# Optimization experiments

Hardware: AMD Instinct MI355X
Metric: run time of the kernel (lower is better)

The kernel has to match this reference:

```python
import jax, jax.numpy as jnp
import numpy as np

# Segmented tensor product, uniform-1d case (subscripts 'u,u,u'):
#   out[z, idx_out[p]*u:(idx_out[p]+1)*u] += coeffs[p] * x0_seg[z, idx0[p]] * x1_seg[z, idx1[p]]
U = 128          # mode extent 'u'
NSEG = (32, 8, 32)  # segments per operand (in0, in1, out)
P = 128          # number of paths
Z = 16384        # batch


def setup_inputs() -> dict:
    key = jax.random.key(0)
    k0, k1, k2, k3, k4, k5 = jax.random.split(key, 6)
    return {
        "x0": jax.random.normal(k0, (Z, NSEG[0] * U), dtype=jnp.float32),
        "x1": jax.random.normal(k1, (Z, NSEG[1] * U), dtype=jnp.float32),
        "coeffs": jax.random.normal(k2, (P,), dtype=jnp.float32),
        "idx0": jax.random.randint(k3, (P,), 0, NSEG[0], dtype=jnp.int32),
        "idx1": jax.random.randint(k4, (P,), 0, NSEG[1], dtype=jnp.int32),
        "idx_out": jax.random.randint(k5, (P,), 0, NSEG[2], dtype=jnp.int32),
    }


def reference(x0, x1, coeffs, idx0, idx1, idx_out):
    z = x0.shape[0]
    x0r = x0.reshape(z, NSEG[0], U)  # [Z, n0, u]
    x1r = x1.reshape(z, NSEG[1], U)  # [Z, n1, u]
    # gather the segment used by each path: [Z, P, u]
    s0 = x0r[:, idx0, :]
    s1 = x1r[:, idx1, :]
    # per-path contribution, elementwise over u (coefficient subscript is scalar)
    contrib = (s0 * s1) * coeffs[None, :, None]          # [Z, P, u]
    # scatter-add paths into output segments
    contrib = jnp.transpose(contrib, (1, 0, 2))          # [P, Z, u]
    out_seg = jax.ops.segment_sum(contrib, idx_out, num_segments=NSEG[2])  # [n2, Z, u]
    return jnp.transpose(out_seg, (1, 0, 2)).reshape(z, NSEG[2] * U)
```

## Files before the change

kernel.cpp:

```cpp
#include <hip/hip_runtime.h>


#define Z_DIM 16384
#define U_DIM 128
#define NSEG0 32
#define NSEG1 8
#define NSEG2 32
#define P_DIM 128
#define ZPB   2
#define BLK   512
#define NBLOCKS 512
#define NTILES  (Z_DIM / ZPB)
#define TILES_PER_BLOCK (NTILES / NBLOCKS)

#define X0_FLOATS (ZPB * NSEG0 * U_DIM)
#define X1_FLOATS (ZPB * NSEG1 * U_DIM)
#define BUF_FLOATS (X0_FLOATS + X1_FLOATS)

typedef float f32x4 __attribute__((ext_vector_type(4)));

__global__ __launch_bounds__(128) void tp_setup(
    const float* __restrict__ coeffs,
    const int* __restrict__ idx0,
    const int* __restrict__ idx1,
    const int* __restrict__ idx_out,
    int* __restrict__ off_g,
    int2* __restrict__ meta_g)
{
    __shared__ int s_cnt[NSEG2];
    __shared__ int s_off[NSEG2 + 1];
    const int t = threadIdx.x;
    if (t < NSEG2) s_cnt[t] = 0;
    __syncthreads();
    const int o = idx_out[t];
    const int r = atomicAdd(&s_cnt[o], 1);
    __syncthreads();
    if (t == 0) {
        int sum = 0;
        for (int i = 0; i < NSEG2; ++i) { s_off[i] = sum; sum += s_cnt[i]; }
        s_off[NSEG2] = sum;
    }
    __syncthreads();
    meta_g[s_off[o] + r] = make_int2((idx0[t] * (U_DIM * 4)) | ((idx1[t] * (U_DIM * 4)) << 16),
                                     __float_as_int(coeffs[t]));
    if (t <= NSEG2) off_g[t] = s_off[t];
}

__device__ __forceinline__ void stage_tile(const float* __restrict__ x0,
                                           const float* __restrict__ x1,
                                           float* lbuf, size_t z0, int t)
{
    const float4* g0 = reinterpret_cast<const float4*>(x0 + z0 * (NSEG0 * U_DIM));
    const float4* g1 = reinterpret_cast<const float4*>(x1 + z0 * (NSEG1 * U_DIM));
    float4* l0 = reinterpret_cast<float4*>(lbuf);
    float4* l1 = reinterpret_cast<float4*>(lbuf + X0_FLOATS);
    #pragma unroll
    for (int i = 0; i < (X0_FLOATS / 4) / BLK; ++i)
        __builtin_amdgcn_global_load_lds(
            (const __attribute__((address_space(1))) void*)(g0 + i * BLK + t),
            (__attribute__((address_space(3))) void*)(l0 + i * BLK + t),
            16, 0, 0);
    __builtin_amdgcn_global_load_lds(
        (const __attribute__((address_space(1))) void*)(g1 + t),
        (__attribute__((address_space(3))) void*)(l1 + t),
        16, 0, 0);
}

__global__ __launch_bounds__(BLK) void tp_kernel(
    const float* __restrict__ x0,
    const float* __restrict__ x1,
    const int* __restrict__ off_g,
    const int2* __restrict__ meta_g,
    float* __restrict__ out)
{
    __shared__ float buf[2][BUF_FLOATS];

    const int t  = threadIdx.x;
    const int w4 = __builtin_amdgcn_readfirstlane(t >> 6) * 4;
    const int zl = (t >> 5) & 1;
    const int uq = t & 31;

    const size_t tile0 = (size_t)blockIdx.x * TILES_PER_BLOCK;

    stage_tile(x0, x1, &buf[0][0], tile0 * ZPB, t);

    int cur = 0;
    for (int i = 0; i < TILES_PER_BLOCK; ++i) {
        __syncthreads();

        if (i + 1 < TILES_PER_BLOCK)
            stage_tile(x0, x1, &buf[cur ^ 1][0], (tile0 + i + 1) * ZPB, t);

        const float* x0base = &buf[cur][zl * (NSEG0 * U_DIM) + uq * 4];
        const float* x1base = &buf[cur][X0_FLOATS + zl * (NSEG1 * U_DIM) + uq * 4];
        const size_t z = (tile0 + i) * ZPB + zl;
        float* orow = out + z * (NSEG2 * U_DIM) + uq * 4;

        #pragma unroll
        for (int oo = 0; oo < 4; ++oo) {
            const int o = w4 + oo;
            const int b = off_g[o];
            const int e = off_g[o + 1];
            f32x4 acc = (f32x4)0.f;
            for (int k = b; k < e; ++k) {
                const int2  m = meta_g[k];
                const float c = __int_as_float(m.y);
                const f32x4 a = *reinterpret_cast<const f32x4*>(
                    reinterpret_cast<const char*>(x0base) + (m.x & 0xffff));
                const f32x4 v = *reinterpret_cast<const f32x4*>(
                    reinterpret_cast<const char*>(x1base) + ((unsigned)m.x >> 16));
                acc += a * v * c;
            }
            __builtin_nontemporal_store(acc, reinterpret_cast<f32x4*>(orow + o * U_DIM));
        }
        cur ^= 1;
    }
}

extern "C" void kernel_launch(void* const* d_in, const int* in_sizes, int n_in,
                              void* d_out, int out_size, void* d_ws, size_t ws_size,
                              hipStream_t stream) {
    const float* x0      = (const float*)d_in[0];
    const float* x1      = (const float*)d_in[1];
    const float* coeffs  = (const float*)d_in[2];
    const int*   idx0    = (const int*)d_in[3];
    const int*   idx1    = (const int*)d_in[4];
    const int*   idx_out = (const int*)d_in[5];
    float* out = (float*)d_out;

    int*  off_g  = (int*)d_ws;
    int2* meta_g = (int2*)((char*)d_ws + 256);

    tp_setup<<<1, P_DIM, 0, stream>>>(coeffs, idx0, idx1, idx_out, off_g, meta_g);
    tp_kernel<<<NBLOCKS, BLK, 0, stream>>>(x0, x1, off_g, meta_g, out);
}
```

Measured before the change: 122.7 us.

## Launch one block per two-row tile and stage path metadata in LDS

Replaces the persistent double-buffered loop (512 blocks each walking 16 tiles) with one 1024-thread block per two-row tile. Each wave now handles two output segments instead of four, and occupancy is left to the hardware scheduler. The setup kernel writes offsets and path metadata into one padded blob, which each block copies into LDS with global_load_lds, so the inner loop reads LDS instead of global memory and prefetches the next metadata entry. The trade is the loss of explicit load/compute overlap within a block, plus a full barrier and a metadata reload in every one of 8192 blocks.

```diff
diff --git a/kernel.cpp b/kernel.cpp
--- a/kernel.cpp
+++ b/kernel.cpp
@@ -8,14 +8,13 @@
 #define NSEG2 32
 #define P_DIM 128
 #define ZPB   2
-#define BLK   512
-#define NBLOCKS 512
-#define NTILES  (Z_DIM / ZPB)
-#define TILES_PER_BLOCK (NTILES / NBLOCKS)
+#define BLK   1024
 
 #define X0_FLOATS (ZPB * NSEG0 * U_DIM)
 #define X1_FLOATS (ZPB * NSEG1 * U_DIM)
-#define BUF_FLOATS (X0_FLOATS + X1_FLOATS)
+
+#define META_BASE 40
+#define BLOB_INTS 304
 
 typedef float f32x4 __attribute__((ext_vector_type(4)));
 
@@ -24,8 +23,7 @@
     const int* __restrict__ idx0,
     const int* __restrict__ idx1,
     const int* __restrict__ idx_out,
-    int* __restrict__ off_g,
-    int2* __restrict__ meta_g)
+    int* __restrict__ blob)
 {
     __shared__ int s_cnt[NSEG2];
     __shared__ int s_off[NSEG2 + 1];
@@ -41,79 +39,80 @@
         s_off[NSEG2] = sum;
     }
     __syncthreads();
-    meta_g[s_off[o] + r] = make_int2((idx0[t] * (U_DIM * 4)) | ((idx1[t] * (U_DIM * 4)) << 16),
-                                     __float_as_int(coeffs[t]));
-    if (t <= NSEG2) off_g[t] = s_off[t];
+    const int d = s_off[o] + r;
+    int2* meta = reinterpret_cast<int2*>(blob + META_BASE);
+    meta[d] = make_int2((idx0[t] * (U_DIM * 4)) | ((idx1[t] * (U_DIM * 4)) << 16),
+                        __float_as_int(coeffs[t]));
+    if (t <= NSEG2) blob[t] = s_off[t];
+    if (t >= 33 && t < META_BASE) blob[t] = 0;
+    if (t >= P_DIM - 8) blob[BLOB_INTS - (P_DIM - t) * 1 - 0] = 0;
 }
 
-__device__ __forceinline__ void stage_tile(const float* __restrict__ x0,
-                                           const float* __restrict__ x1,
-                                           float* lbuf, size_t z0, int t)
-{
-    const float4* g0 = reinterpret_cast<const float4*>(x0 + z0 * (NSEG0 * U_DIM));
-    const float4* g1 = reinterpret_cast<const float4*>(x1 + z0 * (NSEG1 * U_DIM));
-    float4* l0 = reinterpret_cast<float4*>(lbuf);
-    float4* l1 = reinterpret_cast<float4*>(lbuf + X0_FLOATS);
-    #pragma unroll
-    for (int i = 0; i < (X0_FLOATS / 4) / BLK; ++i)
-        __builtin_amdgcn_global_load_lds(
-            (const __attribute__((address_space(1))) void*)(g0 + i * BLK + t),
-            (__attribute__((address_space(3))) void*)(l0 + i * BLK + t),
-            16, 0, 0);
-    __builtin_amdgcn_global_load_lds(
-        (const __attribute__((address_space(1))) void*)(g1 + t),
-        (__attribute__((address_space(3))) void*)(l1 + t),
-        16, 0, 0);
-}
-
-__global__ __launch_bounds__(BLK) void tp_kernel(
+__global__ __launch_bounds__(BLK, 8) void tp_kernel(
     const float* __restrict__ x0,
     const float* __restrict__ x1,
-    const int* __restrict__ off_g,
-    const int2* __restrict__ meta_g,
+    const int* __restrict__ blob_g,
     float* __restrict__ out)
 {
-    __shared__ float buf[2][BUF_FLOATS];
+    __shared__ float s_x0[X0_FLOATS];
+    __shared__ float s_x1[X1_FLOATS];
+    __shared__ int   s_blob[BLOB_INTS];
 
-    const int t  = threadIdx.x;
-    const int w4 = __builtin_amdgcn_readfirstlane(t >> 6) * 4;
+    const int t = threadIdx.x;
+    const size_t z0 = (size_t)blockIdx.x * ZPB;
+
+    {
+        const float4* g0 = reinterpret_cast<const float4*>(x0 + z0 * (NSEG0 * U_DIM));
+        const float4* g1 = reinterpret_cast<const float4*>(x1 + z0 * (NSEG1 * U_DIM));
+        const float4* gb = reinterpret_cast<const float4*>(blob_g);
+        float4* l0 = reinterpret_cast<float4*>(s_x0);
+        float4* l1 = reinterpret_cast<float4*>(s_x1);
+        float4* lb = reinterpret_cast<float4*>(s_blob);
+        #pragma unroll
+        for (int i = 0; i < (X0_FLOATS / 4) / BLK; ++i)
+            __builtin_amdgcn_global_load_lds(
+                (const __attribute__((address_space(1))) void*)(g0 + i * BLK + t),
+                (__attribute__((address_space(3))) void*)(l0 + i * BLK + t),
+                16, 0, 0);
+        if (t < X1_FLOATS / 4)
+            __builtin_amdgcn_global_load_lds(
+                (const __attribute__((address_space(1))) void*)(g1 + t),
+                (__attribute__((address_space(3))) void*)(l1 + t),
+                16, 0, 0);
+        if (t < BLOB_INTS / 4)
+            __builtin_amdgcn_global_load_lds(
+                (const __attribute__((address_space(1))) void*)(gb + t),
+                (__attribute__((address_space(3))) void*)(lb + t),
+                16, 0, 0);
+    }
+    __syncthreads();
+
+    const int w  = t >> 6;
     const int zl = (t >> 5) & 1;
     const int uq = t & 31;
 
-    const size_t tile0 = (size_t)blockIdx.x * TILES_PER_BLOCK;
+    const char* x0base = reinterpret_cast<const char*>(s_x0 + zl * (NSEG0 * U_DIM) + uq * 4);
+    const char* x1base = reinterpret_cast<const char*>(s_x1 + zl * (NSEG1 * U_DIM) + uq * 4);
+    const int2* s_meta = reinterpret_cast<const int2*>(s_blob + META_BASE);
+    const size_t z = z0 + zl;
+    float* orow = out + z * (NSEG2 * U_DIM) + uq * 4;
 
-    stage_tile(x0, x1, &buf[0][0], tile0 * ZPB, t);
-
-    int cur = 0;
-    for (int i = 0; i < TILES_PER_BLOCK; ++i) {
-        __syncthreads();
-
-        if (i + 1 < TILES_PER_BLOCK)
-            stage_tile(x0, x1, &buf[cur ^ 1][0], (tile0 + i + 1) * ZPB, t);
-
-        const float* x0base = &buf[cur][zl * (NSEG0 * U_DIM) + uq * 4];
-        const float* x1base = &buf[cur][X0_FLOATS + zl * (NSEG1 * U_DIM) + uq * 4];
-        const size_t z = (tile0 + i) * ZPB + zl;
-        float* orow = out + z * (NSEG2 * U_DIM) + uq * 4;
-
-        #pragma unroll
-        for (int oo = 0; oo < 4; ++oo) {
-            const int o = w4 + oo;
-            const int b = off_g[o];
-            const int e = off_g[o + 1];
-            f32x4 acc = (f32x4)0.f;
-            for (int k = b; k < e; ++k) {
-                const int2  m = meta_g[k];
-                const float c = __int_as_float(m.y);
-                const f32x4 a = *reinterpret_cast<const f32x4*>(
-                    reinterpret_cast<const char*>(x0base) + (m.x & 0xffff));
-                const f32x4 v = *reinterpret_cast<const f32x4*>(
-                    reinterpret_cast<const char*>(x1base) + ((unsigned)m.x >> 16));
-                acc += a * v * c;
-            }
-            __builtin_nontemporal_store(acc, reinterpret_cast<f32x4*>(orow + o * U_DIM));
+    #pragma unroll
+    for (int oo = 0; oo < 2; ++oo) {
+        const int o = w * 2 + oo;
+        const int b = __builtin_amdgcn_readfirstlane(s_blob[o]);
+        const int e = __builtin_amdgcn_readfirstlane(s_blob[o + 1]);
+        f32x4 acc = (f32x4)0.f;
+        int2 m = s_meta[b];
+        for (int k = b; k < e; ++k) {
+            const int2 mn = s_meta[k + 1];
+            const float c = __int_as_float(m.y);
+            const f32x4 a = *reinterpret_cast<const f32x4*>(x0base + (m.x & 0xffff));
+            const f32x4 v = *reinterpret_cast<const f32x4*>(x1base + ((unsigned)m.x >> 16));
+            acc += a * v * c;
+            m = mn;
         }
-        cur ^= 1;
+        __builtin_nontemporal_store(acc, reinterpret_cast<f32x4*>(orow + o * U_DIM));
     }
 }
 
@@ -128,9 +127,8 @@
     const int*   idx_out = (const int*)d_in[5];
     float* out = (float*)d_out;
 
-    int*  off_g  = (int*)d_ws;
-    int2* meta_g = (int2*)((char*)d_ws + 256);
+    int* blob = (int*)d_ws;
 
-    tp_setup<<<1, P_DIM, 0, stream>>>(coeffs, idx0, idx1, idx_out, off_g, meta_g);
-    tp_kernel<<<NBLOCKS, BLK, 0, stream>>>(x0, x1, off_g, meta_g, out);
+    tp_setup<<<1, P_DIM, 0, stream>>>(coeffs, idx0, idx1, idx_out, blob);
+    tp_kernel<<<Z_DIM / ZPB, BLK, 0, stream>>>(x0, x1, blob, out);
 }
```

Result: faster. 111.1 us (-9.5%).
